# Performance work log

Hardware: AMD Instinct MI355X
Metric: run time of the kernel (lower is better)

Reference implementation:

```python
import jax, jax.numpy as jnp
import numpy as np

NEG_SLOPE = 0.01  # jax.nn.leaky_relu default

def bicubic_resize(x, target_h, target_w):
    # NHWC bicubic resize with antialiasing (matches original module)
    b, h, w, c = x.shape
    return jax.image.resize(x, shape=(b, target_h, target_w, c), method='bicubic', antialias=True)

def setup_inputs() -> dict:
    key = jax.random.key(0)
    x = jax.random.normal(key, (16, 128, 128, 128), dtype=jnp.float32)  # NHWC
    return {"x": x, "in_size": 128, "out_size": 128}

def reference(x, in_size, out_size):
    y = bicubic_resize(x, 2 * in_size, 2 * in_size)
    # activation on the fine grid
    y = jax.nn.leaky_relu(y, negative_slope=NEG_SLOPE)
    # downsample (antialiased) back to out_size
    y = bicubic_resize(y, out_size, out_size)
    return y
```

## Files before the change

### kernel.cpp

```cpp
#include <hip/hip_runtime.h>


typedef float f2 __attribute__((ext_vector_type(2)));

#define HH 128
#define WW 128
#define CC 128
#define RS 16
#define CH 16
#define PADF2 130
#define NSTEP (RS + 4)

__device__ __forceinline__ double keys_cubic(double x) {
  if (x >= 2.0) return 0.0;
  if (x >= 1.0) return ((-0.5 * x + 2.5) * x - 4.0) * x + 2.0;
  return (1.5 * x - 2.5) * x * x + 1.0;
}

__global__ __launch_bounds__(256) void fused_updown_kernel(
    const float* __restrict__ x, float* __restrict__ out) {
  __shared__ __align__(16) float wUpV[256][4];
  __shared__ __align__(16) float wDnE[4][8];
  __shared__ __align__(16) f2 rowv[2][CH][PADF2];

  const int tid = threadIdx.x;

  {
    const int k = tid;
    const double q = 0.5 * k - 0.25;
    const int st = ((k + 1) >> 1) - 2;
    double wr[4], s = 0.0;
#pragma unroll
    for (int i = 0; i < 4; ++i) {
      const int col = st + i;
      double w = (col >= 0 && col <= 127) ? keys_cubic(fabs((double)col - q)) : 0.0;
      wr[i] = w; s += w;
    }
    const double inv = 1.0 / s;
#pragma unroll
    for (int i = 0; i < 4; ++i) wUpV[k][i] = (float)(wr[i] * inv);
  }
  if (tid < 4) {
    const int e = tid;
    const int j = (e < 2) ? e : 124 + e;
    const double p = 2.0 * j + 0.5;
    const int st = 2 * j - 3;
    double wr[8], s = 0.0;
#pragma unroll
    for (int i = 0; i < 8; ++i) {
      const int col = st + i;
      double w = (col >= 0 && col <= 255) ? keys_cubic(0.5 * fabs((double)col - p)) : 0.0;
      wr[i] = w; s += w;
    }
    const double inv = 1.0 / s;
#pragma unroll
    for (int i = 0; i < 8; ++i) wDnE[e][i] = (float)(wr[i] * inv);
  }
  __syncthreads();

  const int bid = blockIdx.x;
  const int b = bid & 15;
  const int strip = (bid >> 4) & 7;
  const int chunk = bid >> 7;
  const int oy0 = strip * RS;
  const int c0 = chunk * CH;
  const int c = tid & 15;
  const int g = tid >> 4;
  const int col0 = g * 8;
  const bool gL = (g == 0), gR = (g == 15);

  const float* xbase = x + (size_t)b * (HH * WW * CC) + (size_t)col0 * CC + (c0 + c);
  float* obase = out + (size_t)b * (HH * WW * CC) + (size_t)col0 * CC + (c0 + c);
  const int m0 = oy0 - 2;

  auto load_row = [&](float (&d)[8], int row) {
    row = row < 0 ? 0 : (row > 127 ? 127 : row);
    const float* p = xbase + (size_t)row * (WW * CC);
#pragma unroll
    for (int j = 0; j < 8; ++j) d[j] = p[j * CC];
  };

  auto wdGet = [&](int oy, float cst, int tap) -> float {
    if (oy < 0 || oy > 127) return 0.f;
    if (oy < 2) return wDnE[oy][tap];
    if (oy > 125) return wDnE[oy - 124][tap];
    return cst;
  };

  float r0[8], r1[8], r2[8], r3[8], r4[8], r5[8];
  float A0[8], A1[8], A2[8], A3[8], A4[8];
#pragma unroll
  for (int i = 0; i < 8; ++i) { A0[i]=0.f; A1[i]=0.f; A2[i]=0.f; A3[i]=0.f; A4[i]=0.f; }

  load_row(r0, m0 - 2);
  load_row(r1, m0 - 1);
  load_row(r2, m0);
  load_row(r3, m0 + 1);
  load_row(r4, m0 + 2);
  load_row(r5, m0 + 3);

  for (int t = 0; t < NSTEP; ++t) {
    const int m = m0 + t;
    if (t > 0) {
#pragma unroll
      for (int i = 0; i < 8; ++i) {
        r0[i]=r1[i]; r1[i]=r2[i]; r2[i]=r3[i]; r3[i]=r4[i]; r4[i]=r5[i];
      }
      load_row(r5, m + 3);
    }
    const bool mOK = (m >= 0) && (m <= 127);
    const int sp = t & 1;
    f2 vown[8];
    if (mOK) {
      const float4 we = *(const float4*)wUpV[2 * m];
      const float4 wo = *(const float4*)wUpV[2 * m + 1];
#pragma unroll
      for (int j = 0; j < 8; ++j) {
        vown[j].x = fmaf(we.x, r0[j], fmaf(we.y, r1[j], fmaf(we.z, r2[j], we.w * r3[j])));
        vown[j].y = fmaf(wo.x, r1[j], fmaf(wo.y, r2[j], fmaf(wo.z, r3[j], wo.w * r4[j])));
      }
#pragma unroll
      for (int j = 0; j < 8; ++j) rowv[sp][c][col0 + j] = vown[j];
    }
    __syncthreads();
    if (mOK) {
      f2 vv[16];
      if (!gL) {
#pragma unroll
        for (int i = 0; i < 4; ++i) vv[i] = rowv[sp][c][col0 - 4 + i];
      } else {
#pragma unroll
        for (int i = 0; i < 4; ++i) vv[i] = f2{0.f, 0.f};
      }
#pragma unroll
      for (int j = 0; j < 8; ++j) vv[4 + j] = vown[j];
      if (!gR) {
#pragma unroll
        for (int i = 0; i < 4; ++i) vv[12 + i] = rowv[sp][c][col0 + 8 + i];
      } else {
#pragma unroll
        for (int i = 0; i < 4; ++i) vv[12 + i] = f2{0.f, 0.f};
      }

      f2 ff[22];
#pragma unroll
      for (int u = 0; u < 22; ++u) {
        const int s = (u >> 1) + 1;
        f2 t2;
        if (u & 1)
          t2 = vv[s] * (-0.0234375f) + vv[s + 1] * 0.2265625f
             + vv[s + 2] * 0.8671875f + vv[s + 3] * (-0.0703125f);
        else
          t2 = vv[s] * (-0.0703125f) + vv[s + 1] * 0.8671875f
             + vv[s + 2] * 0.2265625f + vv[s + 3] * (-0.0234375f);
        ff[u] = __builtin_elementwise_max(t2, t2 * 0.01f);
      }
      if (gL) {
#pragma unroll
        for (int u = 3; u <= 5; ++u) {
          const int s = (u >> 1) + 1;
          const float4 w = *(const float4*)wUpV[u - 3];
          f2 t2 = vv[s] * w.x + vv[s + 1] * w.y + vv[s + 2] * w.z + vv[s + 3] * w.w;
          ff[u] = __builtin_elementwise_max(t2, t2 * 0.01f);
        }
      }
      if (gR) {
#pragma unroll
        for (int u = 16; u <= 18; ++u) {
          const int s = (u >> 1) + 1;
          const float4 w = *(const float4*)wUpV[237 + u];
          f2 t2 = vv[s] * w.x + vv[s + 1] * w.y + vv[s + 2] * w.z + vv[s + 3] * w.w;
          ff[u] = __builtin_elementwise_max(t2, t2 * 0.01f);
        }
      }

      f2 tt[8];
#pragma unroll
      for (int jj = 0; jj < 8; ++jj) {
        tt[jj] = (ff[2*jj]     + ff[2*jj + 7]) * (-0.01171875f)
               + (ff[2*jj + 1] + ff[2*jj + 6]) * (-0.03515625f)
               + (ff[2*jj + 2] + ff[2*jj + 5]) * 0.11328125f
               + (ff[2*jj + 3] + ff[2*jj + 4]) * 0.43359375f;
      }
      if (gL) {
#pragma unroll
        for (int jj = 0; jj < 2; ++jj) {
          f2 s2 = f2{0.f, 0.f};
#pragma unroll
          for (int i = 0; i < 8; ++i) s2 += ff[2*jj + i] * wDnE[jj][i];
          tt[jj] = s2;
        }
      }
      if (gR) {
#pragma unroll
        for (int jj = 6; jj < 8; ++jj) {
          f2 s2 = f2{0.f, 0.f};
#pragma unroll
          for (int i = 0; i < 8; ++i) s2 += ff[2*jj + i] * wDnE[jj - 4][i];
          tt[jj] = s2;
        }
      }

      const float wE0 = wdGet(m - 2, -0.01171875f, 7);
      const float wE1 = wdGet(m - 1, 0.11328125f, 5);
      const float wE2 = wdGet(m, 0.43359375f, 3);
      const float wE3 = wdGet(m + 1, -0.03515625f, 1);
      const float wO0 = wdGet(m - 1, -0.03515625f, 6);
      const float wO1 = wdGet(m, 0.43359375f, 4);
      const float wO2 = wdGet(m + 1, 0.11328125f, 2);
      const float wO3 = wdGet(m + 2, -0.01171875f, 0);
#pragma unroll
      for (int jj = 0; jj < 8; ++jj) {
        const float te = tt[jj].x, to = tt[jj].y;
        A0[jj] = fmaf(wE0, te, A0[jj]);
        A1[jj] = fmaf(wE1, te, fmaf(wO0, to, A1[jj]));
        A2[jj] = fmaf(wE2, te, fmaf(wO1, to, A2[jj]));
        A3[jj] = fmaf(wE3, te, fmaf(wO2, to, A3[jj]));
        A4[jj] = fmaf(wO3, to, A4[jj]);
      }
    }
    if (m - 2 >= oy0) {
      float* op = obase + (size_t)(m - 2) * (WW * CC);
#pragma unroll
      for (int jj = 0; jj < 8; ++jj) op[jj * CC] = A0[jj];
    }
#pragma unroll
    for (int jj = 0; jj < 8; ++jj) {
      A0[jj]=A1[jj]; A1[jj]=A2[jj]; A2[jj]=A3[jj]; A3[jj]=A4[jj]; A4[jj]=0.f;
    }
  }
}

extern "C" void kernel_launch(void* const* d_in, const int* in_sizes, int n_in,
                              void* d_out, int out_size, void* d_ws, size_t ws_size,
                              hipStream_t stream) {
  const float* x = (const float*)d_in[0];
  float* o = (float*)d_out;
  dim3 grid(16 * 8 * 8);
  dim3 block(256);
  hipLaunchKernelGGL(fused_updown_kernel, grid, block, 0, stream, x, o);
}
```

Before: 106.2 us.

## Process two rows per barrier pair and rotate register windows by renaming

Restructures the row loop so each iteration handles two coarse rows. Both upsampled rows are written to the two shared-memory slots, and both are then processed between a pair of lightweight barriers. The register row window and the accumulator rotation are done by renaming macro arguments in a 3x-unrolled loop instead of copying registers. Shared-memory reads and writes become float4 vectors, and the own-column values are re-read from LDS. This is meant to cut barrier count, register moves and LDS instruction count. The cost is more code and higher register pressure, with a second barrier per pair.

```diff
diff --git a/kernel.cpp b/kernel.cpp
--- a/kernel.cpp
+++ b/kernel.cpp
@@ -9,7 +9,8 @@
 #define RS 16
 #define CH 16
 #define PADF2 130
-#define NSTEP (RS + 4)
+
+#define LBAR() asm volatile("s_waitcnt lgkmcnt(0)\n\ts_barrier" ::: "memory")
 
 __device__ __forceinline__ double keys_cubic(double x) {
   if (x >= 2.0) return 0.0;
@@ -87,11 +88,153 @@
     return cst;
   };
 
+#define PROC(SL, Mv, P0, P1, P2, P3, P4) do {                                  \
+    f2 vv[16];                                                                 \
+    if (!gL) {                                                                 \
+      *(float4*)&vv[0] = *(const float4*)&rowv[SL][c][col0 - 4];               \
+      *(float4*)&vv[2] = *(const float4*)&rowv[SL][c][col0 - 2];               \
+    } else {                                                                   \
+      vv[0] = f2{0.f,0.f}; vv[1] = f2{0.f,0.f};                                \
+      vv[2] = f2{0.f,0.f}; vv[3] = f2{0.f,0.f};                                \
+    }                                                                          \
+    *(float4*)&vv[4]  = *(const float4*)&rowv[SL][c][col0];                    \
+    *(float4*)&vv[6]  = *(const float4*)&rowv[SL][c][col0 + 2];                \
+    *(float4*)&vv[8]  = *(const float4*)&rowv[SL][c][col0 + 4];                \
+    *(float4*)&vv[10] = *(const float4*)&rowv[SL][c][col0 + 6];                \
+    if (!gR) {                                                                 \
+      *(float4*)&vv[12] = *(const float4*)&rowv[SL][c][col0 + 8];              \
+      *(float4*)&vv[14] = *(const float4*)&rowv[SL][c][col0 + 10];             \
+    } else {                                                                   \
+      vv[12] = f2{0.f,0.f}; vv[13] = f2{0.f,0.f};                              \
+      vv[14] = f2{0.f,0.f}; vv[15] = f2{0.f,0.f};                              \
+    }                                                                          \
+    f2 ff[22];                                                                 \
+    _Pragma("unroll") for (int u = 0; u < 22; ++u) {                           \
+      const int s = (u >> 1) + 1;                                              \
+      f2 t2;                                                                   \
+      if (u & 1)                                                               \
+        t2 = vv[s] * (-0.0234375f) + vv[s + 1] * 0.2265625f                    \
+           + vv[s + 2] * 0.8671875f + vv[s + 3] * (-0.0703125f);               \
+      else                                                                     \
+        t2 = vv[s] * (-0.0703125f) + vv[s + 1] * 0.8671875f                    \
+           + vv[s + 2] * 0.2265625f + vv[s + 3] * (-0.0234375f);               \
+      ff[u] = __builtin_elementwise_max(t2, t2 * 0.01f);                       \
+    }                                                                          \
+    if (gL) {                                                                  \
+      _Pragma("unroll") for (int u = 3; u <= 5; ++u) {                         \
+        const int s = (u >> 1) + 1;                                            \
+        const float4 w = *(const float4*)wUpV[u - 3];                          \
+        f2 t2 = vv[s] * w.x + vv[s+1] * w.y + vv[s+2] * w.z + vv[s+3] * w.w;   \
+        ff[u] = __builtin_elementwise_max(t2, t2 * 0.01f);                     \
+      }                                                                        \
+    }                                                                          \
+    if (gR) {                                                                  \
+      _Pragma("unroll") for (int u = 16; u <= 18; ++u) {                       \
+        const int s = (u >> 1) + 1;                                            \
+        const float4 w = *(const float4*)wUpV[237 + u];                        \
+        f2 t2 = vv[s] * w.x + vv[s+1] * w.y + vv[s+2] * w.z + vv[s+3] * w.w;   \
+        ff[u] = __builtin_elementwise_max(t2, t2 * 0.01f);                     \
+      }                                                                        \
+    }                                                                          \
+    f2 tt[8];                                                                  \
+    _Pragma("unroll") for (int jj = 0; jj < 8; ++jj) {                         \
+      tt[jj] = (ff[2*jj]     + ff[2*jj + 7]) * (-0.01171875f)                  \
+             + (ff[2*jj + 1] + ff[2*jj + 6]) * (-0.03515625f)                  \
+             + (ff[2*jj + 2] + ff[2*jj + 5]) * 0.11328125f                     \
+             + (ff[2*jj + 3] + ff[2*jj + 4]) * 0.43359375f;                    \
+    }                                                                          \
+    if (gL) {                                                                  \
+      _Pragma("unroll") for (int jj = 0; jj < 2; ++jj) {                       \
+        f2 s2 = f2{0.f, 0.f};                                                  \
+        _Pragma("unroll") for (int i = 0; i < 8; ++i)                          \
+          s2 += ff[2*jj + i] * wDnE[jj][i];                                    \
+        tt[jj] = s2;                                                           \
+      }                                                                        \
+    }                                                                          \
+    if (gR) {                                                                  \
+      _Pragma("unroll") for (int jj = 6; jj < 8; ++jj) {                       \
+        f2 s2 = f2{0.f, 0.f};                                                  \
+        _Pragma("unroll") for (int i = 0; i < 8; ++i)                          \
+          s2 += ff[2*jj + i] * wDnE[jj - 4][i];                                \
+        tt[jj] = s2;                                                           \
+      }                                                                        \
+    }                                                                          \
+    const float wE0 = wdGet((Mv) - 2, -0.01171875f, 7);                        \
+    const float wE1 = wdGet((Mv) - 1, 0.11328125f, 5);                         \
+    const float wE2 = wdGet((Mv),     0.43359375f, 3);                         \
+    const float wE3 = wdGet((Mv) + 1, -0.03515625f, 1);                        \
+    const float wO0 = wdGet((Mv) - 1, -0.03515625f, 6);                        \
+    const float wO1 = wdGet((Mv),     0.43359375f, 4);                         \
+    const float wO2 = wdGet((Mv) + 1, 0.11328125f, 2);                         \
+    const float wO3 = wdGet((Mv) + 2, -0.01171875f, 0);                        \
+    _Pragma("unroll") for (int jj = 0; jj < 8; ++jj) {                         \
+      const float te = tt[jj].x, to = tt[jj].y;                                \
+      P0[jj] = fmaf(wE0, te, P0[jj]);                                          \
+      P1[jj] = fmaf(wE1, te, fmaf(wO0, to, P1[jj]));                           \
+      P2[jj] = fmaf(wE2, te, fmaf(wO1, to, P2[jj]));                           \
+      P3[jj] = fmaf(wE3, te, fmaf(wO2, to, P3[jj]));                           \
+      P4[jj] = fmaf(wO3, to, P4[jj]);                                          \
+    }                                                                          \
+  } while (0)
+
+#define PAIR(P, Ra,Rb,Rc,Rd,Re,Rf, Aa,Ab,Ac,Ad,Ae,Af) do {                     \
+    const int mA = m0 + 2*(P);                                                 \
+    const int mB = mA + 1;                                                     \
+    const bool mAok = (mA >= 0) && (mA <= 127);                                \
+    const bool mBok = (mB >= 0) && (mB <= 127);                                \
+    if (mAok) {                                                                \
+      const float4 we = *(const float4*)wUpV[2 * mA];                          \
+      const float4 wo = *(const float4*)wUpV[2 * mA + 1];                      \
+      f2 vn[8];                                                                \
+      _Pragma("unroll") for (int j = 0; j < 8; ++j) {                          \
+        vn[j].x = fmaf(we.x, Ra[j], fmaf(we.y, Rb[j],                          \
+                  fmaf(we.z, Rc[j], we.w * Rd[j])));                           \
+        vn[j].y = fmaf(wo.x, Rb[j], fmaf(wo.y, Rc[j],                          \
+                  fmaf(wo.z, Rd[j], wo.w * Re[j])));                           \
+      }                                                                        \
+      *(float4*)&rowv[0][c][col0]     = *(float4*)&vn[0];                      \
+      *(float4*)&rowv[0][c][col0 + 2] = *(float4*)&vn[2];                      \
+      *(float4*)&rowv[0][c][col0 + 4] = *(float4*)&vn[4];                      \
+      *(float4*)&rowv[0][c][col0 + 6] = *(float4*)&vn[6];                      \
+    }                                                                          \
+    if (mBok) {                                                                \
+      const float4 we = *(const float4*)wUpV[2 * mB];                          \
+      const float4 wo = *(const float4*)wUpV[2 * mB + 1];                      \
+      f2 vn[8];                                                                \
+      _Pragma("unroll") for (int j = 0; j < 8; ++j) {                          \
+        vn[j].x = fmaf(we.x, Rb[j], fmaf(we.y, Rc[j],                          \
+                  fmaf(we.z, Rd[j], we.w * Re[j])));                           \
+        vn[j].y = fmaf(wo.x, Rc[j], fmaf(wo.y, Rd[j],                          \
+                  fmaf(wo.z, Re[j], wo.w * Rf[j])));                           \
+      }                                                                        \
+      *(float4*)&rowv[1][c][col0]     = *(float4*)&vn[0];                      \
+      *(float4*)&rowv[1][c][col0 + 2] = *(float4*)&vn[2];                      \
+      *(float4*)&rowv[1][c][col0 + 4] = *(float4*)&vn[4];                      \
+      *(float4*)&rowv[1][c][col0 + 6] = *(float4*)&vn[6];                      \
+    }                                                                          \
+    load_row(Ra, mA + 4);                                                      \
+    load_row(Rb, mA + 5);                                                      \
+    LBAR();                                                                    \
+    if (mAok) PROC(0, mA, Aa, Ab, Ac, Ad, Ae);                                 \
+    if (mBok) PROC(1, mB, Ab, Ac, Ad, Ae, Af);                                 \
+    if (mA - 2 >= oy0) {                                                       \
+      float* op = obase + (size_t)(mA - 2) * (WW * CC);                        \
+      _Pragma("unroll") for (int jj = 0; jj < 8; ++jj) op[jj * CC] = Aa[jj];   \
+    }                                                                          \
+    if (mB - 2 >= oy0) {                                                       \
+      float* op = obase + (size_t)(mB - 2) * (WW * CC);                        \
+      _Pragma("unroll") for (int jj = 0; jj < 8; ++jj) op[jj * CC] = Ab[jj];   \
+    }                                                                          \
+    _Pragma("unroll") for (int jj = 0; jj < 8; ++jj) { Aa[jj]=0.f; Ab[jj]=0.f; } \
+    LBAR();                                                                    \
+  } while (0)
+
   float r0[8], r1[8], r2[8], r3[8], r4[8], r5[8];
-  float A0[8], A1[8], A2[8], A3[8], A4[8];
-#pragma unroll
-  for (int i = 0; i < 8; ++i) { A0[i]=0.f; A1[i]=0.f; A2[i]=0.f; A3[i]=0.f; A4[i]=0.f; }
-
+  float a0[8], a1[8], a2[8], a3[8], a4[8], a5[8];
+#pragma unroll
+  for (int i = 0; i < 8; ++i) {
+    a0[i]=0.f; a1[i]=0.f; a2[i]=0.f; a3[i]=0.f; a4[i]=0.f; a5[i]=0.f;
+  }
   load_row(r0, m0 - 2);
   load_row(r1, m0 - 1);
   load_row(r2, m0);
@@ -99,136 +242,16 @@
   load_row(r4, m0 + 2);
   load_row(r5, m0 + 3);
 
-  for (int t = 0; t < NSTEP; ++t) {
-    const int m = m0 + t;
-    if (t > 0) {
-#pragma unroll
-      for (int i = 0; i < 8; ++i) {
-        r0[i]=r1[i]; r1[i]=r2[i]; r2[i]=r3[i]; r3[i]=r4[i]; r4[i]=r5[i];
-      }
-      load_row(r5, m + 3);
-    }
-    const bool mOK = (m >= 0) && (m <= 127);
-    const int sp = t & 1;
-    f2 vown[8];
-    if (mOK) {
-      const float4 we = *(const float4*)wUpV[2 * m];
-      const float4 wo = *(const float4*)wUpV[2 * m + 1];
-#pragma unroll
-      for (int j = 0; j < 8; ++j) {
-        vown[j].x = fmaf(we.x, r0[j], fmaf(we.y, r1[j], fmaf(we.z, r2[j], we.w * r3[j])));
-        vown[j].y = fmaf(wo.x, r1[j], fmaf(wo.y, r2[j], fmaf(wo.z, r3[j], wo.w * r4[j])));
-      }
-#pragma unroll
-      for (int j = 0; j < 8; ++j) rowv[sp][c][col0 + j] = vown[j];
-    }
-    __syncthreads();
-    if (mOK) {
-      f2 vv[16];
-      if (!gL) {
-#pragma unroll
-        for (int i = 0; i < 4; ++i) vv[i] = rowv[sp][c][col0 - 4 + i];
-      } else {
-#pragma unroll
-        for (int i = 0; i < 4; ++i) vv[i] = f2{0.f, 0.f};
-      }
-#pragma unroll
-      for (int j = 0; j < 8; ++j) vv[4 + j] = vown[j];
-      if (!gR) {
-#pragma unroll
-        for (int i = 0; i < 4; ++i) vv[12 + i] = rowv[sp][c][col0 + 8 + i];
-      } else {
-#pragma unroll
-        for (int i = 0; i < 4; ++i) vv[12 + i] = f2{0.f, 0.f};
-      }
-
-      f2 ff[22];
-#pragma unroll
-      for (int u = 0; u < 22; ++u) {
-        const int s = (u >> 1) + 1;
-        f2 t2;
-        if (u & 1)
-          t2 = vv[s] * (-0.0234375f) + vv[s + 1] * 0.2265625f
-             + vv[s + 2] * 0.8671875f + vv[s + 3] * (-0.0703125f);
-        else
-          t2 = vv[s] * (-0.0703125f) + vv[s + 1] * 0.8671875f
-             + vv[s + 2] * 0.2265625f + vv[s + 3] * (-0.0234375f);
-        ff[u] = __builtin_elementwise_max(t2, t2 * 0.01f);
-      }
-      if (gL) {
-#pragma unroll
-        for (int u = 3; u <= 5; ++u) {
-          const int s = (u >> 1) + 1;
-          const float4 w = *(const float4*)wUpV[u - 3];
-          f2 t2 = vv[s] * w.x + vv[s + 1] * w.y + vv[s + 2] * w.z + vv[s + 3] * w.w;
-          ff[u] = __builtin_elementwise_max(t2, t2 * 0.01f);
-        }
-      }
-      if (gR) {
-#pragma unroll
-        for (int u = 16; u <= 18; ++u) {
-          const int s = (u >> 1) + 1;
-          const float4 w = *(const float4*)wUpV[237 + u];
-          f2 t2 = vv[s] * w.x + vv[s + 1] * w.y + vv[s + 2] * w.z + vv[s + 3] * w.w;
-          ff[u] = __builtin_elementwise_max(t2, t2 * 0.01f);
-        }
-      }
-
-      f2 tt[8];
-#pragma unroll
-      for (int jj = 0; jj < 8; ++jj) {
-        tt[jj] = (ff[2*jj]     + ff[2*jj + 7]) * (-0.01171875f)
-               + (ff[2*jj + 1] + ff[2*jj + 6]) * (-0.03515625f)
-               + (ff[2*jj + 2] + ff[2*jj + 5]) * 0.11328125f
-               + (ff[2*jj + 3] + ff[2*jj + 4]) * 0.43359375f;
-      }
-      if (gL) {
-#pragma unroll
-        for (int jj = 0; jj < 2; ++jj) {
-          f2 s2 = f2{0.f, 0.f};
-#pragma unroll
-          for (int i = 0; i < 8; ++i) s2 += ff[2*jj + i] * wDnE[jj][i];
-          tt[jj] = s2;
-        }
-      }
-      if (gR) {
-#pragma unroll
-        for (int jj = 6; jj < 8; ++jj) {
-          f2 s2 = f2{0.f, 0.f};
-#pragma unroll
-          for (int i = 0; i < 8; ++i) s2 += ff[2*jj + i] * wDnE[jj - 4][i];
-          tt[jj] = s2;
-        }
-      }
-
-      const float wE0 = wdGet(m - 2, -0.01171875f, 7);
-      const float wE1 = wdGet(m - 1, 0.11328125f, 5);
-      const float wE2 = wdGet(m, 0.43359375f, 3);
-      const float wE3 = wdGet(m + 1, -0.03515625f, 1);
-      const float wO0 = wdGet(m - 1, -0.03515625f, 6);
-      const float wO1 = wdGet(m, 0.43359375f, 4);
-      const float wO2 = wdGet(m + 1, 0.11328125f, 2);
-      const float wO3 = wdGet(m + 2, -0.01171875f, 0);
-#pragma unroll
-      for (int jj = 0; jj < 8; ++jj) {
-        const float te = tt[jj].x, to = tt[jj].y;
-        A0[jj] = fmaf(wE0, te, A0[jj]);
-        A1[jj] = fmaf(wE1, te, fmaf(wO0, to, A1[jj]));
-        A2[jj] = fmaf(wE2, te, fmaf(wO1, to, A2[jj]));
-        A3[jj] = fmaf(wE3, te, fmaf(wO2, to, A3[jj]));
-        A4[jj] = fmaf(wO3, to, A4[jj]);
-      }
-    }
-    if (m - 2 >= oy0) {
-      float* op = obase + (size_t)(m - 2) * (WW * CC);
-#pragma unroll
-      for (int jj = 0; jj < 8; ++jj) op[jj * CC] = A0[jj];
-    }
-#pragma unroll
-    for (int jj = 0; jj < 8; ++jj) {
-      A0[jj]=A1[jj]; A1[jj]=A2[jj]; A2[jj]=A3[jj]; A3[jj]=A4[jj]; A4[jj]=0.f;
-    }
-  }
+  for (int i = 0; i < 3; ++i) {
+    const int p = 3 * i;
+    PAIR(p,     r0,r1,r2,r3,r4,r5, a0,a1,a2,a3,a4,a5);
+    PAIR(p + 1, r2,r3,r4,r5,r0,r1, a2,a3,a4,a5,a0,a1);
+    PAIR(p + 2, r4,r5,r0,r1,r2,r3, a4,a5,a0,a1,a2,a3);
+  }
+  PAIR(9, r0,r1,r2,r3,r4,r5, a0,a1,a2,a3,a4,a5);
+
+#undef PAIR
+#undef PROC
 }
 
 extern "C" void kernel_launch(void* const* d_in, const int* in_sizes, int n_in,
```

Measured after the change: 122.6 us. +15.4%, slower.
